# Optimization experiments

Hardware: AMD Instinct MI355X
Metric: run time of the kernel (lower is better)

## Reference

```python
import jax, jax.numpy as jnp
import numpy as np

GAMMA = 1.0
CONNECTIVITY_WEIGHT = 0.001


def setup_inputs() -> dict:
    key = jax.random.key(0)
    k1, k2 = jax.random.split(key)
    B, C, P, L = 65536, 2, 41, 4
    logits = jax.random.normal(k1, (B, C, P, L), dtype=jnp.float32)
    targets = jax.random.randint(k2, (B, P, L), 0, C, dtype=jnp.int64)
    return {"logits": logits, "targets": targets}


def compute_boundary_weights(labels, alpha=GAMMA):
    # labels: [B, P, L] int -> float boundary weights [B, P, L]
    beta = alpha * 0.5
    lab = labels.astype(jnp.float32)
    diff1 = jnp.abs(lab[:, 1:, :] - lab[:, :-1, :])   # [B, P-1, L]
    diff2 = jnp.abs(lab[:, 2:, :] - lab[:, :-2, :])   # [B, P-2, L]
    w = jnp.zeros_like(lab)
    w = w.at[:, 1:, :].add(alpha * diff1)
    w = w.at[:, :-1, :].add(alpha * diff1)
    w = w.at[:, 2:, :].add(beta * diff2)
    w = w.at[:, :-2, :].add(beta * diff2)
    return w + 1.0


def reference(logits, targets):
    # logits: [B, C, P, L], targets: [B, P, L]
    # Cross-entropy over class dim (axis=1), reduction='none'
    logp = jax.nn.log_softmax(logits, axis=1)                      # [B, C, P, L]
    loss_ce = -jnp.take_along_axis(logp, targets[:, None, :, :], axis=1)[:, 0]  # [B, P, L]

    weights = compute_boundary_weights(targets, GAMMA)
    weighted_loss_ce = loss_ce * weights

    # Connectivity: 1 where consecutive predicted classes differ (point 0 -> 0)
    pred = jnp.argmax(logits, axis=1)                              # [B, P, L]
    diff = (pred[:, 1:, :] != pred[:, :-1, :]).astype(loss_ce.dtype)
    connectivity = jnp.concatenate(
        [jnp.zeros_like(diff[:, :1, :]), diff], axis=1)            # [B, P, L]

    total = weighted_loss_ce + CONNECTIVITY_WEIGHT * connectivity
    return jnp.mean(total)
```

## Files before the change

kernel.cpp:

```cpp
#include <hip/hip_runtime.h>

constexpr int B    = 65536;
constexpr int P    = 41;
constexpr int NTH  = B * P;
constexpr int NBLK = NTH / 256;
constexpr float INV_N = 1.0f / (float)(B * P * 4);
constexpr float CW    = 0.001f;

__device__ __forceinline__ float comp1(float l0, float l1, float q0, float q1,
                                       int tx, int am1, int ap1, int am2, int ap2)
{
    float d  = l1 - l0;
    float g  = __logf(1.0f + __expf(-fabsf(d)));
    float ft = (float)tx;
    float sd = d * fmaf(-2.0f, ft, 1.0f);
    float ce = fmaxf(sd, 0.0f) + g;

    int   x1 = (tx ^ am1) + (tx ^ ap1);
    int   x2 = (tx ^ am2) + (tx ^ ap2);
    float w  = fmaf(0.5f, (float)x2, 1.0f + (float)x1);

    float dm   = q1 - q0;
    float conn = ((d > 0.0f) != (dm > 0.0f)) ? CW : 0.0f;
    return fmaf(ce, w, conn);
}

__global__ __launch_bounds__(256)
void lace_partial_kernel(const float4* __restrict__ lg4,
                         const int4*   __restrict__ tg4,
                         float*        __restrict__ partial)
{
    const int t = blockIdx.x * 256 + threadIdx.x;
    const int b = t / P;
    const int p = t - b * P;

    const int pm1 = (p >= 1) ? p - 1 : p;
    const int pp1 = (p <= P - 2) ? p + 1 : p;
    const int pm2 = (p >= 2) ? p - 2 : p;
    const int pp2 = (p <= P - 3) ? p + 2 : p;

    const int f4 = b * 82 + p;
    const int fm = b * 82 + pm1;
    const int tb = t - p;

    float4 a0 = lg4[f4];
    float4 a1 = lg4[f4 + 41];
    float4 q0 = lg4[fm];
    float4 q1 = lg4[fm + 41];
    int4   tc = tg4[t];
    int4   nA = tg4[tb + pm1];
    int4   nB = tg4[tb + pp1];
    int4   nC = tg4[tb + pm2];
    int4   nD = tg4[tb + pp2];

    float sum = comp1(a0.x, a1.x, q0.x, q1.x, tc.x, nA.x, nB.x, nC.x, nD.x)
              + comp1(a0.y, a1.y, q0.y, q1.y, tc.y, nA.y, nB.y, nC.y, nD.y)
              + comp1(a0.z, a1.z, q0.z, q1.z, tc.z, nA.z, nB.z, nC.z, nD.z)
              + comp1(a0.w, a1.w, q0.w, q1.w, tc.w, nA.w, nB.w, nC.w, nD.w);

    #pragma unroll
    for (int off = 32; off > 0; off >>= 1)
        sum += __shfl_down(sum, off, 64);

    __shared__ float wsum[4];
    const int lane = threadIdx.x & 63;
    const int wid  = threadIdx.x >> 6;
    if (lane == 0) wsum[wid] = sum;
    __syncthreads();
    if (threadIdx.x == 0)
        partial[blockIdx.x] = wsum[0] + wsum[1] + wsum[2] + wsum[3];
}

__global__ __launch_bounds__(1024)
void lace_reduce_kernel(const float* __restrict__ partial,
                        float*       __restrict__ out)
{
    float s = 0.0f;
    for (int i = threadIdx.x; i < NBLK; i += 1024)
        s += partial[i];

    #pragma unroll
    for (int off = 32; off > 0; off >>= 1)
        s += __shfl_down(s, off, 64);

    __shared__ float wsum[16];
    const int lane = threadIdx.x & 63;
    const int wid  = threadIdx.x >> 6;
    if (lane == 0) wsum[wid] = s;
    __syncthreads();
    if (threadIdx.x == 0) {
        float total = 0.0f;
        #pragma unroll
        for (int i = 0; i < 16; ++i) total += wsum[i];
        out[0] = total * INV_N;
    }
}

extern "C" void kernel_launch(void* const* d_in, const int* in_sizes, int n_in,
                              void* d_out, int out_size, void* d_ws, size_t ws_size,
                              hipStream_t stream) {
    const float4* lg4 = (const float4*)d_in[0];
    const int4*   tg4 = (const int4*)d_in[1];
    float* out     = (float*)d_out;
    float* partial = (float*)d_ws;

    lace_partial_kernel<<<NBLK, 256, 0, stream>>>(lg4, tg4, partial);
    lace_reduce_kernel<<<1, 1024, 0, stream>>>(partial, out);
}
```

Before: 155.6 us.

## Stage neighbor targets and logit diffs in shared memory instead of redundant global loads

Each thread now loads only its own logits and targets and writes them into shared-memory tiles with a small halo. Neighbor targets (p±1, p±2) and the previous point's logit difference are then read from LDS rather than issued as extra global loads. This cuts per-thread global requests from nine to three, at the cost of a block barrier and some LDS traffic. The final reduction kernel also switches to float4 loads of the partial sums.

Result: no change. 158.2 us (+1.7%).

```diff
diff --git a/kernel.cpp b/kernel.cpp
--- a/kernel.cpp
+++ b/kernel.cpp
@@ -3,14 +3,14 @@
 constexpr int B    = 65536;
 constexpr int P    = 41;
 constexpr int NTH  = B * P;
-constexpr int NBLK = NTH / 256;
+constexpr int BLK  = 256;
+constexpr int NBLK = NTH / BLK;
 constexpr float INV_N = 1.0f / (float)(B * P * 4);
 constexpr float CW    = 0.001f;
 
-__device__ __forceinline__ float comp1(float l0, float l1, float q0, float q1,
-                                       int tx, int am1, int ap1, int am2, int ap2)
+__device__ __forceinline__ float comp1(float d, float dm, int tx,
+                                       int am1, int ap1, int am2, int ap2)
 {
-    float d  = l1 - l0;
     float g  = __logf(1.0f + __expf(-fabsf(d)));
     float ft = (float)tx;
     float sd = d * fmaf(-2.0f, ft, 1.0f);
@@ -20,7 +20,6 @@
     int   x2 = (tx ^ am2) + (tx ^ ap2);
     float w  = fmaf(0.5f, (float)x2, 1.0f + (float)x1);
 
-    float dm   = q1 - q0;
     float conn = ((d > 0.0f) != (dm > 0.0f)) ? CW : 0.0f;
     return fmaf(ce, w, conn);
 }
@@ -30,33 +29,58 @@
                          const int4*   __restrict__ tg4,
                          float*        __restrict__ partial)
 {
-    const int t = blockIdx.x * 256 + threadIdx.x;
-    const int b = t / P;
-    const int p = t - b * P;
+    __shared__ int4   stg[BLK + 4];
+    __shared__ float4 sdv[BLK + 1];
 
-    const int pm1 = (p >= 1) ? p - 1 : p;
-    const int pp1 = (p <= P - 2) ? p + 1 : p;
-    const int pm2 = (p >= 2) ? p - 2 : p;
-    const int pp2 = (p <= P - 3) ? p + 2 : p;
-
-    const int f4 = b * 82 + p;
-    const int fm = b * 82 + pm1;
-    const int tb = t - p;
+    const int tid = threadIdx.x;
+    const int t   = blockIdx.x * BLK + tid;
+    const int b   = t / P;
+    const int p   = t - b * P;
+    const int f4  = b * 82 + p;
 
     float4 a0 = lg4[f4];
     float4 a1 = lg4[f4 + 41];
-    float4 q0 = lg4[fm];
-    float4 q1 = lg4[fm + 41];
     int4   tc = tg4[t];
-    int4   nA = tg4[tb + pm1];
-    int4   nB = tg4[tb + pp1];
-    int4   nC = tg4[tb + pm2];
-    int4   nD = tg4[tb + pp2];
 
-    float sum = comp1(a0.x, a1.x, q0.x, q1.x, tc.x, nA.x, nB.x, nC.x, nD.x)
-              + comp1(a0.y, a1.y, q0.y, q1.y, tc.y, nA.y, nB.y, nC.y, nD.y)
-              + comp1(a0.z, a1.z, q0.z, q1.z, tc.z, nA.z, nB.z, nC.z, nD.z)
-              + comp1(a0.w, a1.w, q0.w, q1.w, tc.w, nA.w, nB.w, nC.w, nD.w);
+    if (tid < 2)        stg[tid]     = tg4[max(t - 2, 0)];
+    if (tid >= BLK - 2) stg[tid + 4] = tg4[min(t + 2, NTH - 1)];
+    if (tid == 0) {
+        const int tm = max(t - 1, 0);
+        const int bm = tm / P;
+        const int pm = tm - bm * P;
+        const int fm = bm * 82 + pm;
+        float4 q0 = lg4[fm];
+        float4 q1 = lg4[fm + 41];
+        float4 dh;
+        dh.x = q1.x - q0.x; dh.y = q1.y - q0.y;
+        dh.z = q1.z - q0.z; dh.w = q1.w - q0.w;
+        sdv[0] = dh;
+    }
+
+    float4 d4;
+    d4.x = a1.x - a0.x; d4.y = a1.y - a0.y;
+    d4.z = a1.z - a0.z; d4.w = a1.w - a0.w;
+
+    stg[tid + 2] = tc;
+    sdv[tid + 1] = d4;
+    __syncthreads();
+
+    const int om1 = (p >= 1)     ? 1 : 0;
+    const int op1 = (p <= P - 2) ? 1 : 0;
+    const int om2 = (p >= 2)     ? 2 : 0;
+    const int op2 = (p <= P - 3) ? 2 : 0;
+
+    const int li = tid + 2;
+    const int4   nA = stg[li - om1];
+    const int4   nB = stg[li + op1];
+    const int4   nC = stg[li - om2];
+    const int4   nD = stg[li + op2];
+    const float4 dm = sdv[tid + 1 - om1];
+
+    float sum = comp1(d4.x, dm.x, tc.x, nA.x, nB.x, nC.x, nD.x)
+              + comp1(d4.y, dm.y, tc.y, nA.y, nB.y, nC.y, nD.y)
+              + comp1(d4.z, dm.z, tc.z, nA.z, nB.z, nC.z, nD.z)
+              + comp1(d4.w, dm.w, tc.w, nA.w, nB.w, nC.w, nD.w);
 
     #pragma unroll
     for (int off = 32; off > 0; off >>= 1)
@@ -72,12 +96,15 @@
 }
 
 __global__ __launch_bounds__(1024)
-void lace_reduce_kernel(const float* __restrict__ partial,
-                        float*       __restrict__ out)
+void lace_reduce_kernel(const float4* __restrict__ partial4,
+                        float*        __restrict__ out)
 {
+    constexpr int N4 = NBLK / 4;
     float s = 0.0f;
-    for (int i = threadIdx.x; i < NBLK; i += 1024)
-        s += partial[i];
+    for (int i = threadIdx.x; i < N4; i += 1024) {
+        float4 v = partial4[i];
+        s += (v.x + v.y) + (v.z + v.w);
+    }
 
     #pragma unroll
     for (int off = 32; off > 0; off >>= 1)
@@ -105,5 +132,5 @@
     float* partial = (float*)d_ws;
 
     lace_partial_kernel<<<NBLK, 256, 0, stream>>>(lg4, tg4, partial);
-    lace_reduce_kernel<<<1, 1024, 0, stream>>>(partial, out);
+    lace_reduce_kernel<<<1, 1024, 0, stream>>>((const float4*)partial, out);
 }
```
